# Optimization experiments

Hardware: AMD Instinct MI355X
Metric: run time of the kernel (lower is better)

The kernel has to match this reference:

```python
import jax, jax.numpy as jnp
import numpy as np

NB_ATOMS = 128
NB_CH = 1
ATOM = 12          # atom_size
BATCH = 8
HW = 75            # -> 64x64 patch grid
LAM = 0.1          # soft-threshold level of the L1 proximal
UNROLL = 2         # unroll_steps
FISTA_ITERS = 15   # fixed inner FISTA iterations (replaces res-based stop)


def _prox(u):
    # soft-thresholding (prox of lam*||.||_1)
    return jnp.sign(u) * jnp.maximum(jnp.abs(u) - LAM, 0.0)


def _conv(x, w):
    # valid cross-correlation, NCHW / OIHW (== F.conv2d)
    return jax.lax.conv_general_dilated(x, w, (1, 1), 'VALID',
                                        dimension_numbers=('NCHW', 'OIHW', 'NCHW'))


def _fold(patches, H, W):
    # patches: [B, Ph, Pw, a, a] -> overlap-add to [B, 1, H, W] (== F.fold)
    B, Ph, Pw, a, _ = patches.shape
    out = jnp.zeros((B, H, W), patches.dtype)
    for di in range(a):              # fixed small kernel loop (a*a = 144 slots)
        for dj in range(a):
            out = out.at[:, di:di + Ph, dj:dj + Pw].add(patches[:, :, :, di, dj])
    return out[:, None]


def _fista(c0, X, q, mu):
    # standard FISTA on 0.5*||D^T c - y_patch||^2 + lam*||c||_1 with step mu
    def body(i, st):
        c, z, t = st
        cn = _prox(z - (z @ X - q) * mu)
        tn = (1.0 + jnp.sqrt(1.0 + 4.0 * t * t)) / 2.0
        zn = cn + ((t - 1.0) / tn) * (cn - c)
        return (cn, zn, tn)
    c, _, _ = jax.lax.fori_loop(0, FISTA_ITERS, body, (c0, c0, jnp.float32(1.0)))
    return c


def setup_inputs() -> dict:
    key = jax.random.key(0)
    k1, k2 = jax.random.split(key)
    y = jax.random.normal(k1, (BATCH, NB_CH, HW, HW), dtype=jnp.float32)
    atoms = jax.random.normal(k2, (NB_ATOMS, NB_CH, ATOM, ATOM), dtype=jnp.float32) / 1500.0
    beta = jnp.float32(0.1)
    mu = jnp.float32(1.0)
    return {"y": y, "atoms": atoms, "beta": beta, "mu": mu}


def reference(y, atoms, beta, mu):
    B, C, H, W = y.shape
    N, a = atoms.shape[0], atoms.shape[-1]
    beta = jax.nn.relu(beta)
    mu = jax.nn.relu(mu)
    # normalize atoms: zero-mean, unit L2 rows, then spectral norm / sqrt(mu)
    A = atoms - atoms.mean(axis=(1, 2, 3), keepdims=True)
    Af = A.reshape(N, -1)
    Af = Af / jnp.linalg.norm(Af, axis=1, keepdims=True)
    Af = Af / (jnp.linalg.norm(Af, ord=2) * jnp.sqrt(mu))
    atoms_n = Af.reshape(N, C, a, a)
    X = Af @ Af.T                                   # [N, N] gram
    Ph, Pw = H - a + 1, W - a + 1
    n_patch = B * Ph * Pw
    mean_filter = jnp.ones((1, 1, a, a), y.dtype) / (a * a)
    patch_mean = _conv(y, mean_filter).reshape(n_patch, 1, 1, 1)
    divisors = _fold(jnp.ones((B, Ph, Pw, a, a), y.dtype), H, W)  # overlap counts
    goal = y
    c = jnp.zeros((n_patch, N), y.dtype)
    sg = jax.lax.stop_gradient
    for _ in range(UNROLL):
        q = _conv(goal, atoms_n).transpose(0, 2, 3, 1).reshape(n_patch, N)
        cf = sg(_fista(sg(c), sg(X), sg(q), sg(mu)))   # torch.no_grad inner solve
        cf = _prox(cf - (cf @ X - q) * mu)             # one differentiable step
        pred = jnp.einsum('pn,ncij->pcij', cf, atoms_n) + patch_mean  # [P,1,a,a]
        pred = _fold(pred.reshape(B, Ph, Pw, a, a), H, W)
        goal = (y + beta * pred) / (1.0 + beta * divisors)
        c = cf
    return goal
```

## Files before the change

### kernel.cpp

```cpp
#include <hip/hip_runtime.h>
#include <stdint.h>

#define AA 144
#define LAM 0.1f

#define OFS_SC    0
#define OFS_AF1   64
#define OFS_G     36928
#define OFS_S0    53312
#define OFS_S1    69696
#define OFS_X     86080
#define OFS_PM    139328
#define OFS_GOAL  172096
#define OFS_CF    4411456
#define OFS_PRED  8605760
#define OFS_ATB   OFS_S0
#define OFS_ANTB  OFS_S1


typedef __attribute__((ext_vector_type(8))) short short8_t;
typedef __attribute__((ext_vector_type(4))) float f32x4;
typedef __attribute__((ext_vector_type(2))) float f32x2;
typedef __attribute__((ext_vector_type(4))) uint32_t u32x4;

__device__ __forceinline__ unsigned short f2bf(float f) {
    union { float f; uint32_t u; } x; x.f = f;
    uint32_t u = x.u;
    return (unsigned short)((u + 0x7FFFu + ((u >> 16) & 1u)) >> 16);
}
__device__ __forceinline__ unsigned short f2bh(float f) {
    union { float f; uint32_t u; } x; x.f = f;
    return (unsigned short)((x.u + 0x8000u) >> 16);
}
__device__ __forceinline__ float bf2f(unsigned short u) {
    union { float f; uint32_t i; } x; x.i = ((uint32_t)u) << 16; return x.f;
}
__device__ __forceinline__ uint32_t pack_bf(float a, float b) {
    union { float f; uint32_t u; } xa, xb; xa.f = a; xb.f = b;
    return __builtin_amdgcn_perm(xb.u + 0x8000u, xa.u + 0x8000u, 0x07060302u);
}
__device__ __forceinline__ uint32_t cvt_pk(float a, float b) {
    uint32_t r;
    asm("v_cvt_pk_bf16_f32 %0, %1, %2" : "=v"(r) : "v"(a), "v"(b));
    return r;
}

#define PSTR 136
__global__ __launch_bounds__(1024) void k_setup(const float* atoms, const float* mu_p,
                                                float* ws, const float* y) {
    __shared__ unsigned short ABf[128 * 168];
    __shared__ unsigned short Pb[2][128 * PSTR];
    __shared__ float tr_arr[10];
    __shared__ float v[128];
    __shared__ float red[256];
    int t = threadIdx.x;
    if (blockIdx.x != 0) {
        int e = (blockIdx.x - 1) * 1024 + t;
        if (e < 45000) ws[OFS_GOAL + e] = y[e];
        if (e < 32768) {
            int b = e >> 12, pi = (e >> 6) & 63, pj = e & 63;
            const float* yb = y + b * 5625;
            float s = 0.f;
            for (int di = 0; di < 12; ++di) {
                const float* row = yb + (pi + di) * 75 + pj;
                #pragma unroll
                for (int dj = 0; dj < 12; ++dj) s += row[dj];
            }
            ws[OFS_PM + e] = s * (1.0f / 144.0f);
        }
        return;
    }
    int lane = t & 63, w = t >> 6;
    int col = lane & 15, quad = lane >> 4;
    if (t < 10) tr_arr[t] = (t == 0) ? 128.0f : 0.f;

    {
        int a = t >> 3, sub = t & 7;
        const float* ap = atoms + a * AA + sub * 18;
        float s = 0.f;
        #pragma unroll
        for (int k = 0; k < 18; ++k) s += ap[k];
        s += __shfl_xor(s, 1, 8); s += __shfl_xor(s, 2, 8); s += __shfl_xor(s, 4, 8);
        float mean = s * (1.0f / 144.0f);
        float ss = 0.f;
        #pragma unroll
        for (int k = 0; k < 18; ++k) { float d = ap[k] - mean; ss = fmaf(d, d, ss); }
        ss += __shfl_xor(ss, 1, 8); ss += __shfl_xor(ss, 2, 8); ss += __shfl_xor(ss, 4, 8);
        float rn = 1.0f / sqrtf(ss);
        #pragma unroll
        for (int k = 0; k < 18; ++k) {
            float av = (ap[k] - mean) * rn;
            ws[OFS_AF1 + a * AA + sub * 18 + k] = av;
            ABf[a * 168 + sub * 18 + k] = f2bf(av);
        }
        if (sub == 0) {
            #pragma unroll
            for (int k = AA; k < 160; ++k) ABf[a * 168 + k] = 0;
        }
    }
    __syncthreads();

    {
        uint32_t* D32 = (uint32_t*)Pb[0];
        float* G = ws + OFS_G;
        int mt = w & 7, gh = w >> 3;
        short8_t af[5];
        #pragma unroll
        for (int s = 0; s < 5; ++s)
            af[s] = *(const short8_t*)&ABf[(mt * 16 + col) * 168 + s * 32 + quad * 8];
        #pragma unroll
        for (int gi = 0; gi < 2; ++gi) {
            int g = gh * 2 + gi;
            short8_t b0[5], b1[5];
            #pragma unroll
            for (int s = 0; s < 5; ++s) {
                b0[s] = *(const short8_t*)&ABf[((2 * g) * 16 + col) * 168 + s * 32 + quad * 8];
                b1[s] = *(const short8_t*)&ABf[((2 * g + 1) * 16 + col) * 168 + s * 32 + quad * 8];
            }
            f32x4 a0 = (f32x4){0.f, 0.f, 0.f, 0.f};
            f32x4 a1 = (f32x4){0.f, 0.f, 0.f, 0.f};
            #pragma unroll
            for (int s = 0; s < 5; ++s) {
                a0 = __builtin_amdgcn_mfma_f32_16x16x32_bf16(af[s], b0[s], a0, 0, 0, 0);
                a1 = __builtin_amdgcn_mfma_f32_16x16x32_bf16(af[s], b1[s], a1, 0, 0, 0);
            }
            #pragma unroll
            for (int r = 0; r < 4; ++r) {
                int m = mt * 16 + quad * 4 + r;
                G[m * 128 + g * 32 + col] = a0[r];
                G[m * 128 + g * 32 + 16 + col] = a1[r];
                D32[m * 68 + g * 16 + col] = pack_bf(a0[r], a1[r]);
            }
        }
    }
    __syncthreads();

    int cur = 0;
    #pragma unroll 1
    for (int j = 0; j < 8; ++j) {
        float trn = tr_arr[j];
        float inv2 = 1.0f / (trn * trn);
        const unsigned short* S = Pb[cur];
        uint32_t* D32 = (uint32_t*)Pb[cur ^ 1];
        int mt = w & 7, nh = w >> 3;
        short8_t af[4];
        #pragma unroll
        for (int s = 0; s < 4; ++s)
            af[s] = *(const short8_t*)&S[(mt * 16 + col) * PSTR + s * 32 + quad * 8];
        #pragma unroll
        for (int pr = 0; pr < 2; ++pr) {
            int ntE = 4 * nh + 2 * pr, ntO = ntE + 1;
            short8_t bE[4], bO[4];
            #pragma unroll
            for (int s = 0; s < 4; ++s) {
                bE[s] = *(const short8_t*)&S[(ntE * 16 + col) * PSTR + s * 32 + quad * 8];
                bO[s] = *(const short8_t*)&S[(ntO * 16 + col) * PSTR + s * 32 + quad * 8];
            }
            f32x4 aE = (f32x4){0.f, 0.f, 0.f, 0.f};
            f32x4 aO = (f32x4){0.f, 0.f, 0.f, 0.f};
            #pragma unroll
            for (int s = 0; s < 4; ++s) {
                aE = __builtin_amdgcn_mfma_f32_16x16x32_bf16(af[s], bE[s], aE, 0, 0, 0);
                aO = __builtin_amdgcn_mfma_f32_16x16x32_bf16(af[s], bO[s], aO, 0, 0, 0);
            }
            int nE = ntE * 16 + col, nO = ntO * 16 + col;
            #pragma unroll
            for (int r = 0; r < 4; ++r) {
                float x0 = aE[r] * inv2, x1 = aO[r] * inv2;
                int row = mt * 16 + quad * 4 + r;
                D32[row * 68 + (ntE >> 1) * 16 + col] = pack_bf(x0, x1);
                if (row == nE) atomicAdd(&tr_arr[j + 1], x0);
                if (row == nO) atomicAdd(&tr_arr[j + 1], x1);
            }
        }
        __syncthreads();
        cur ^= 1;
    }

    {
        int a = t >> 3, sub = t & 7;
        const unsigned short* S = Pb[cur];
        float s = 0.f;
        #pragma unroll
        for (int k = 0; k < 16; ++k) s += bf2f(S[a * PSTR + sub * 16 + k]);
        s += __shfl_xor(s, 1, 8); s += __shfl_xor(s, 2, 8); s += __shfl_xor(s, 4, 8);
        if (sub == 0) v[a] = s;
    }
    __syncthreads();
    {
        int a = t >> 3, sub = t & 7;
        const float* G = ws + OFS_G;
        float wv = 0.f;
        #pragma unroll
        for (int k = 0; k < 16; ++k)
            wv = fmaf(G[a * 128 + sub * 16 + k], v[sub * 16 + k], wv);
        wv += __shfl_xor(wv, 1, 8); wv += __shfl_xor(wv, 2, 8); wv += __shfl_xor(wv, 4, 8);
        if (sub == 0) { red[a] = v[a] * wv; red[128 + a] = v[a] * v[a]; }
    }
    __syncthreads();
    for (int off = 64; off > 0; off >>= 1) {
        if (t < off) { red[t] += red[t + off]; red[128 + t] += red[128 + t + off]; }
        __syncthreads();
    }
    if (t == 0) {
        float lam = red[0] / red[128];
        float mu = fmaxf(mu_p[0], 0.0f);
        float scX = 1.0f / (lam * mu);
        float scA = 1.0f / (sqrtf(lam) * sqrtf(mu));
        ws[OFS_SC + 16] = scX * mu;
        ws[OFS_SC + 17] = scA;
        ws[OFS_SC + 18] = -scA * mu;
    }
}

__global__ __launch_bounds__(256) void k_finalize(float* ws) {
    int idx = blockIdx.x * 256 + threadIdx.x;
    float scX = ws[OFS_SC + 16], scA = ws[OFS_SC + 17], scQ = ws[OFS_SC + 18];
    if (idx < 16384) {
        int row = idx >> 7, ks = idx & 127;
        int s = ks >> 5, Q = (ks >> 3) & 3, j = ks & 7;
        int n = 32 * s + 16 * (j >> 2) + 4 * Q + (j & 3);
        ((unsigned short*)(ws + OFS_X))[idx] = f2bf(ws[OFS_G + row * 128 + n] * scX);
    } else if (idx < 36864) {
        int e = idx - 16384;
        int n = e / 160, k = e - n * 160;
        float v = (k < 144) ? ws[OFS_AF1 + n * 144 + k] * scQ : 0.f;
        ((unsigned short*)(ws + OFS_ATB))[e] = f2bf(v);
    } else {
        int e = idx - 36864;
        int jr = e >> 7, ks = e & 127;
        int s = ks >> 5, Q = (ks >> 3) & 3, j = ks & 7;
        int n = 32 * s + 16 * (j >> 2) + 4 * Q + (j & 3);
        ((unsigned short*)(ws + OFS_ANTB))[e] = f2bf(ws[OFS_AF1 + n * 144 + jr] * scA);
    }
}

__global__ __launch_bounds__(64, 1) void k_fista(const unsigned short* XPB,
        const float* goal, const unsigned short* ATB, const unsigned short* ANTBP,
        const float* pm, uint32_t* cfgb, unsigned short* predh,
        int first, int write_cf) {
    int lane = threadIdx.x & 63;
    int col = lane & 15, Q = lane >> 4;
    int wid = blockIdx.x;
    int b = wid >> 8, pi = (wid >> 2) & 63;
    int pcol = (wid & 3) * 16 + col;
    int p = wid * 16 + col;
    const float* gb = goal + b * 5625 + pi * 75;

    u32x4 bq[5];
    #pragma unroll
    for (int s = 0; s < 5; ++s)
        #pragma unroll
        for (int jj = 0; jj < 4; ++jj) {
            int k0 = 32 * s + 8 * Q + 2 * jj;
            float v0 = 0.f, v1 = 0.f;
            if (k0 < 144) {
                int di = k0 / 12, dj = k0 - di * 12;
                const float* r = gb + di * 75 + pcol + dj;
                v0 = r[0]; v1 = r[1];
            }
            bq[s][jj] = cvt_pk(v0, v1);
        }

    f32x4 qn4[8];
    #pragma unroll
    for (int m = 0; m < 8; ++m) {
        short8_t af[5];
        #pragma unroll
        for (int s = 0; s < 5; ++s)
            af[s] = *(const short8_t*)&ATB[(m * 16 + col) * 160 + 32 * s + 8 * Q];
        f32x4 a = (f32x4){0.f, 0.f, 0.f, 0.f};
        #pragma unroll
        for (int s = 0; s < 5; ++s)
            a = __builtin_amdgcn_mfma_f32_16x16x32_bf16(af[s],
                    __builtin_bit_cast(short8_t, bq[s]), a, 0, 0, 0);
        qn4[m] = a;
    }

    short8_t xf[8][4];
    #pragma unroll
    for (int m = 0; m < 8; ++m)
        #pragma unroll
        for (int s = 0; s < 4; ++s)
            xf[m][s] = *(const short8_t*)&XPB[(m * 16 + col) * 128 + 32 * s + 8 * Q];

    f32x4 c4[8], z4[8], acc4[8];
    u32x4 bfr[4];
    if (first) {
        #pragma unroll
        for (int m = 0; m < 8; ++m) c4[m] = z4[m] = (f32x4){0.f, 0.f, 0.f, 0.f};
        #pragma unroll
        for (int s = 0; s < 4; ++s) bfr[s] = (u32x4){0u, 0u, 0u, 0u};
    } else {
        const u32x4* cp = (const u32x4*)(cfgb + ((size_t)wid * 64 + lane) * 16);
        #pragma unroll
        for (int s = 0; s < 4; ++s) {
            u32x4 v = cp[s];
            bfr[s] = v;
            #pragma unroll
            for (int jj = 0; jj < 4; ++jj) {
                int m = (s << 1) | (jj >> 1), r = 2 * (jj & 1);
                uint32_t pk = v[jj];
                c4[m][r]     = __builtin_bit_cast(float, pk << 16);
                c4[m][r + 1] = __builtin_bit_cast(float, pk & 0xFFFF0000u);
            }
        }
        #pragma unroll
        for (int m = 0; m < 8; ++m) z4[m] = c4[m];
    }

    const f32x4 lamP = (f32x4){LAM, LAM, LAM, LAM};
    const f32x4 lamN = (f32x4){-LAM, -LAM, -LAM, -LAM};

    auto matmul = [&]() {
        #pragma unroll
        for (int m = 0; m < 8; ++m)
            acc4[m] = __builtin_amdgcn_mfma_f32_16x16x32_bf16(xf[m][0],
                          __builtin_bit_cast(short8_t, bfr[0]), qn4[m], 0, 0, 0);
        #pragma unroll
        for (int s = 1; s < 4; ++s)
            #pragma unroll
            for (int m = 0; m < 8; ++m)
                acc4[m] = __builtin_amdgcn_mfma_f32_16x16x32_bf16(xf[m][s],
                              __builtin_bit_cast(short8_t, bfr[s]), acc4[m], 0, 0, 0);
    };
    auto pack = [&](f32x4 (&src)[8]) {
        #pragma unroll
        for (int s = 0; s < 4; ++s)
            #pragma unroll
            for (int jj = 0; jj < 4; ++jj) {
                int m = (s << 1) | (jj >> 1), r = 2 * (jj & 1);
                bfr[s][jj] = cvt_pk(src[m][r], src[m][r + 1]);
            }
    };

    float tm = 1.0f;
    #pragma unroll 2
    for (int it = 0; it < 14; ++it) {
        matmul();
        float tn = 0.5f * (1.0f + sqrtf(1.0f + 4.0f * tm * tm));
        float fm = (tm - 1.0f) / tn;
        tm = tn;
        f32x4 fm4 = (f32x4){fm, fm, fm, fm};
        #pragma unroll
        for (int m = 0; m < 8; ++m) {
            f32x4 u = z4[m] - acc4[m];
            f32x4 cl = __builtin_elementwise_min(__builtin_elementwise_max(u, lamN), lamP);
            f32x4 cn = u - cl;
            z4[m] = cn + fm4 * (cn - c4[m]);
            c4[m] = cn;
        }
        pack(z4);
    }
    {
        matmul();
        #pragma unroll
        for (int m = 0; m < 8; ++m) {
            f32x4 u = z4[m] - acc4[m];
            f32x4 cl = __builtin_elementwise_min(__builtin_elementwise_max(u, lamN), lamP);
            c4[m] = u - cl;
        }
        pack(c4);
    }
    {
        matmul();
        #pragma unroll
        for (int m = 0; m < 8; ++m) {
            f32x4 u = c4[m] - acc4[m];
            f32x4 cl = __builtin_elementwise_min(__builtin_elementwise_max(u, lamN), lamP);
            c4[m] = u - cl;
        }
        pack(c4);
    }
    if (write_cf) {
        u32x4* cp = (u32x4*)(cfgb + ((size_t)wid * 64 + lane) * 16);
        #pragma unroll
        for (int s = 0; s < 4; ++s) cp[s] = bfr[s];
    }

    {
        float pmv = pm[p];
        f32x4 pm4 = (f32x4){pmv, pmv, pmv, pmv};
        #pragma unroll
        for (int jm = 0; jm < 9; ++jm) {
            short8_t anf[4];
            #pragma unroll
            for (int s = 0; s < 4; ++s)
                anf[s] = *(const short8_t*)&ANTBP[(jm * 16 + col) * 128 + 32 * s + 8 * Q];
            f32x4 a = pm4;
            #pragma unroll
            for (int s = 0; s < 4; ++s)
                a = __builtin_amdgcn_mfma_f32_16x16x32_bf16(anf[s],
                        __builtin_bit_cast(short8_t, bfr[s]), a, 0, 0, 0);
            #pragma unroll
            for (int r = 0; r < 4; ++r)
                predh[(jm * 16 + 4 * Q + r) * 32768 + p] = f2bh(a[r]);
        }
    }
}

__global__ __launch_bounds__(256) void k_fold(const float* y, const float* beta_p,
                                              const unsigned short* predh, float* goal,
                                              float* out, int write_out) {
    __shared__ float P[12 * 832];
    int i = blockIdx.x, b = blockIdx.y;
    int t = threadIdx.x;
    for (int di = 0; di < 12; ++di) {
        int pi = i - di;
        if ((unsigned)pi >= 64u) continue;
        int base = (b << 12) + (pi << 6);
        #pragma unroll
        for (int it = 0; it < 3; ++it) {
            int e = t + it * 256;
            int dj = e >> 6, pj = e & 63;
            P[di * 832 + pj * 13 + dj] = bf2f(predh[(di * 12 + dj) * 32768 + base + pj]);
        }
    }
    __syncthreads();
    if (t >= 75) return;
    int j = t;
    float S = 0.f;
    for (int di = 0; di < 12; ++di) {
        if ((unsigned)(i - di) >= 64u) continue;
        const float* Pd = &P[di * 832];
        #pragma unroll
        for (int dj = 0; dj < 12; ++dj) {
            int pj = j - dj;
            if ((unsigned)pj >= 64u) continue;
            S += Pd[pj * 13 + dj];
        }
    }
    int ci = min(i, 11) - max(i - 63, 0) + 1;
    int cj = min(j, 11) - max(j - 63, 0) + 1;
    float beta = fmaxf(beta_p[0], 0.0f);
    int idx = i * 75 + j;
    float yv = y[b * 5625 + idx];
    float g = (yv + beta * S) / (1.0f + beta * (float)(ci * cj));
    if (write_out) out[b * 5625 + idx] = g;
    else           goal[b * 5625 + idx] = g;
}

extern "C" void kernel_launch(void* const* d_in, const int* in_sizes, int n_in,
                              void* d_out, int out_size, void* d_ws, size_t ws_size,
                              hipStream_t stream) {
    const float* y     = (const float*)d_in[0];
    const float* atoms = (const float*)d_in[1];
    const float* beta  = (const float*)d_in[2];
    const float* mu    = (const float*)d_in[3];
    float* out = (float*)d_out;
    float* ws = (float*)d_ws;

    k_setup<<<46, 1024, 0, stream>>>(atoms, mu, ws, y);
    k_finalize<<<216, 256, 0, stream>>>(ws);

    for (int u = 0; u < 2; ++u) {
        k_fista<<<2048, 64, 0, stream>>>((const unsigned short*)(ws + OFS_X),
                                         ws + OFS_GOAL,
                                         (const unsigned short*)(ws + OFS_ATB),
                                         (const unsigned short*)(ws + OFS_ANTB),
                                         ws + OFS_PM, (uint32_t*)(ws + OFS_CF),
                                         (unsigned short*)(ws + OFS_PRED),
                                         u == 0 ? 1 : 0, u == 0 ? 1 : 0);
        k_fold<<<dim3(75, 8), 256, 0, stream>>>(y, beta,
                                                (const unsigned short*)(ws + OFS_PRED),
                                                ws + OFS_GOAL, out, u == 1 ? 1 : 0);
    }
}
```

Before: 204.1 us.

## Split FISTA atom rows across two waves with LDS exchange of iterates

Each FISTA block now runs two wavefronts, each owning half of the 128 atom rows of the Gram matvec, and the two halves exchange the packed bf16 iterate through double-buffered shared memory with a barrier every iteration. This halves per-wave MFMA work and register footprint (allowing more resident waves), and the prediction GEMM is split 5/4 across the waves. The soft-threshold clamp is switched to fmed3. The cost is a __syncthreads and LDS round trip per iteration on the serial dependency chain.

```diff
diff --git a/kernel.cpp b/kernel.cpp
--- a/kernel.cpp
+++ b/kernel.cpp
@@ -235,16 +235,18 @@
     }
 }
 
-__global__ __launch_bounds__(64, 1) void k_fista(const unsigned short* XPB,
+__global__ __launch_bounds__(128, 3) void k_fista(const unsigned short* XPB,
         const float* goal, const unsigned short* ATB, const unsigned short* ANTBP,
         const float* pm, uint32_t* cfgb, unsigned short* predh,
         int first, int write_cf) {
-    int lane = threadIdx.x & 63;
+    __shared__ u32x4 Zx[2][2][2][64];
+    int t = threadIdx.x;
+    int lane = t & 63, w = t >> 6;
     int col = lane & 15, Q = lane >> 4;
-    int wid = blockIdx.x;
-    int b = wid >> 8, pi = (wid >> 2) & 63;
-    int pcol = (wid & 3) * 16 + col;
-    int p = wid * 16 + col;
+    int blk = blockIdx.x;
+    int b = blk >> 8, pi = (blk >> 2) & 63;
+    int pcol = (blk & 3) * 16 + col;
+    int p = blk * 16 + col;
     const float* gb = goal + b * 5625 + pi * 75;
 
     u32x4 bq[5];
@@ -262,13 +264,13 @@
             bq[s][jj] = cvt_pk(v0, v1);
         }
 
-    f32x4 qn4[8];
+    f32x4 qn4[4];
     #pragma unroll
-    for (int m = 0; m < 8; ++m) {
+    for (int m = 0; m < 4; ++m) {
         short8_t af[5];
         #pragma unroll
         for (int s = 0; s < 5; ++s)
-            af[s] = *(const short8_t*)&ATB[(m * 16 + col) * 160 + 32 * s + 8 * Q];
+            af[s] = *(const short8_t*)&ATB[((w * 4 + m) * 16 + col) * 160 + 32 * s + 8 * Q];
         f32x4 a = (f32x4){0.f, 0.f, 0.f, 0.f};
         #pragma unroll
         for (int s = 0; s < 5; ++s)
@@ -277,61 +279,67 @@
         qn4[m] = a;
     }
 
-    short8_t xf[8][4];
+    short8_t xf[4][4];
     #pragma unroll
-    for (int m = 0; m < 8; ++m)
+    for (int m = 0; m < 4; ++m)
         #pragma unroll
         for (int s = 0; s < 4; ++s)
-            xf[m][s] = *(const short8_t*)&XPB[(m * 16 + col) * 128 + 32 * s + 8 * Q];
-
-    f32x4 c4[8], z4[8], acc4[8];
+            xf[m][s] = *(const short8_t*)&XPB[((w * 4 + m) * 16 + col) * 128 + 32 * s + 8 * Q];
+
+    f32x4 c4[4], z4[4], acc4[4];
     u32x4 bfr[4];
     if (first) {
         #pragma unroll
-        for (int m = 0; m < 8; ++m) c4[m] = z4[m] = (f32x4){0.f, 0.f, 0.f, 0.f};
+        for (int m = 0; m < 4; ++m) c4[m] = z4[m] = (f32x4){0.f, 0.f, 0.f, 0.f};
         #pragma unroll
         for (int s = 0; s < 4; ++s) bfr[s] = (u32x4){0u, 0u, 0u, 0u};
     } else {
-        const u32x4* cp = (const u32x4*)(cfgb + ((size_t)wid * 64 + lane) * 16);
-        #pragma unroll
-        for (int s = 0; s < 4; ++s) {
-            u32x4 v = cp[s];
-            bfr[s] = v;
+        const u32x4* cp = (const u32x4*)(cfgb + ((size_t)blk * 64 + lane) * 16);
+        #pragma unroll
+        for (int s = 0; s < 4; ++s) bfr[s] = cp[s];
+        #pragma unroll
+        for (int sp = 0; sp < 2; ++sp) {
+            u32x4 v = bfr[2 * w + sp];
             #pragma unroll
             for (int jj = 0; jj < 4; ++jj) {
-                int m = (s << 1) | (jj >> 1), r = 2 * (jj & 1);
+                int m = (sp << 1) | (jj >> 1), r = 2 * (jj & 1);
                 uint32_t pk = v[jj];
                 c4[m][r]     = __builtin_bit_cast(float, pk << 16);
                 c4[m][r + 1] = __builtin_bit_cast(float, pk & 0xFFFF0000u);
             }
         }
         #pragma unroll
-        for (int m = 0; m < 8; ++m) z4[m] = c4[m];
-    }
-
-    const f32x4 lamP = (f32x4){LAM, LAM, LAM, LAM};
-    const f32x4 lamN = (f32x4){-LAM, -LAM, -LAM, -LAM};
+        for (int m = 0; m < 4; ++m) z4[m] = c4[m];
+    }
 
     auto matmul = [&]() {
         #pragma unroll
-        for (int m = 0; m < 8; ++m)
+        for (int m = 0; m < 4; ++m)
             acc4[m] = __builtin_amdgcn_mfma_f32_16x16x32_bf16(xf[m][0],
                           __builtin_bit_cast(short8_t, bfr[0]), qn4[m], 0, 0, 0);
         #pragma unroll
         for (int s = 1; s < 4; ++s)
             #pragma unroll
-            for (int m = 0; m < 8; ++m)
+            for (int m = 0; m < 4; ++m)
                 acc4[m] = __builtin_amdgcn_mfma_f32_16x16x32_bf16(xf[m][s],
                               __builtin_bit_cast(short8_t, bfr[s]), acc4[m], 0, 0, 0);
     };
-    auto pack = [&](f32x4 (&src)[8]) {
-        #pragma unroll
-        for (int s = 0; s < 4; ++s)
+    auto pack = [&](f32x4 (&src)[4]) {
+        #pragma unroll
+        for (int sp = 0; sp < 2; ++sp)
             #pragma unroll
             for (int jj = 0; jj < 4; ++jj) {
-                int m = (s << 1) | (jj >> 1), r = 2 * (jj & 1);
-                bfr[s][jj] = cvt_pk(src[m][r], src[m][r + 1]);
-            }
+                int m = (sp << 1) | (jj >> 1), r = 2 * (jj & 1);
+                bfr[2 * w + sp][jj] = cvt_pk(src[m][r], src[m][r + 1]);
+            }
+    };
+    int ow = w ^ 1;
+    auto exchange = [&](int buf) {
+        Zx[buf][w][0][lane] = bfr[2 * w];
+        Zx[buf][w][1][lane] = bfr[2 * w + 1];
+        __syncthreads();
+        bfr[2 * ow]     = Zx[buf][ow][0][lane];
+        bfr[2 * ow + 1] = Zx[buf][ow][1][lane];
     };
 
     float tm = 1.0f;
@@ -343,58 +351,71 @@
         tm = tn;
         f32x4 fm4 = (f32x4){fm, fm, fm, fm};
         #pragma unroll
-        for (int m = 0; m < 8; ++m) {
+        for (int m = 0; m < 4; ++m) {
             f32x4 u = z4[m] - acc4[m];
-            f32x4 cl = __builtin_elementwise_min(__builtin_elementwise_max(u, lamN), lamP);
+            f32x4 cl;
+            #pragma unroll
+            for (int e = 0; e < 4; ++e) cl[e] = __builtin_amdgcn_fmed3f(u[e], -LAM, LAM);
             f32x4 cn = u - cl;
             z4[m] = cn + fm4 * (cn - c4[m]);
             c4[m] = cn;
         }
         pack(z4);
+        exchange(it & 1);
     }
     {
         matmul();
         #pragma unroll
-        for (int m = 0; m < 8; ++m) {
+        for (int m = 0; m < 4; ++m) {
             f32x4 u = z4[m] - acc4[m];
-            f32x4 cl = __builtin_elementwise_min(__builtin_elementwise_max(u, lamN), lamP);
+            f32x4 cl;
+            #pragma unroll
+            for (int e = 0; e < 4; ++e) cl[e] = __builtin_amdgcn_fmed3f(u[e], -LAM, LAM);
             c4[m] = u - cl;
         }
         pack(c4);
+        exchange(0);
     }
     {
         matmul();
         #pragma unroll
-        for (int m = 0; m < 8; ++m) {
+        for (int m = 0; m < 4; ++m) {
             f32x4 u = c4[m] - acc4[m];
-            f32x4 cl = __builtin_elementwise_min(__builtin_elementwise_max(u, lamN), lamP);
+            f32x4 cl;
+            #pragma unroll
+            for (int e = 0; e < 4; ++e) cl[e] = __builtin_amdgcn_fmed3f(u[e], -LAM, LAM);
             c4[m] = u - cl;
         }
         pack(c4);
+        exchange(1);
     }
     if (write_cf) {
-        u32x4* cp = (u32x4*)(cfgb + ((size_t)wid * 64 + lane) * 16);
-        #pragma unroll
-        for (int s = 0; s < 4; ++s) cp[s] = bfr[s];
+        u32x4* cp = (u32x4*)(cfgb + ((size_t)blk * 64 + lane) * 16);
+        cp[2 * w]     = bfr[2 * w];
+        cp[2 * w + 1] = bfr[2 * w + 1];
     }
 
     {
         float pmv = pm[p];
         f32x4 pm4 = (f32x4){pmv, pmv, pmv, pmv};
-        #pragma unroll
-        for (int jm = 0; jm < 9; ++jm) {
-            short8_t anf[4];
-            #pragma unroll
-            for (int s = 0; s < 4; ++s)
-                anf[s] = *(const short8_t*)&ANTBP[(jm * 16 + col) * 128 + 32 * s + 8 * Q];
-            f32x4 a = pm4;
-            #pragma unroll
-            for (int s = 0; s < 4; ++s)
-                a = __builtin_amdgcn_mfma_f32_16x16x32_bf16(anf[s],
-                        __builtin_bit_cast(short8_t, bfr[s]), a, 0, 0, 0);
-            #pragma unroll
-            for (int r = 0; r < 4; ++r)
-                predh[(jm * 16 + 4 * Q + r) * 32768 + p] = f2bh(a[r]);
+        int jm0 = w ? 5 : 0, jmN = w ? 4 : 5;
+        #pragma unroll
+        for (int ji = 0; ji < 5; ++ji) {
+            if (ji < jmN) {
+                int jm = jm0 + ji;
+                short8_t anf[4];
+                #pragma unroll
+                for (int s = 0; s < 4; ++s)
+                    anf[s] = *(const short8_t*)&ANTBP[(jm * 16 + col) * 128 + 32 * s + 8 * Q];
+                f32x4 a = pm4;
+                #pragma unroll
+                for (int s = 0; s < 4; ++s)
+                    a = __builtin_amdgcn_mfma_f32_16x16x32_bf16(anf[s],
+                            __builtin_bit_cast(short8_t, bfr[s]), a, 0, 0, 0);
+                #pragma unroll
+                for (int r = 0; r < 4; ++r)
+                    predh[(jm * 16 + 4 * Q + r) * 32768 + p] = f2bh(a[r]);
+            }
         }
     }
 }
@@ -454,13 +475,13 @@
     k_finalize<<<216, 256, 0, stream>>>(ws);
 
     for (int u = 0; u < 2; ++u) {
-        k_fista<<<2048, 64, 0, stream>>>((const unsigned short*)(ws + OFS_X),
-                                         ws + OFS_GOAL,
-                                         (const unsigned short*)(ws + OFS_ATB),
-                                         (const unsigned short*)(ws + OFS_ANTB),
-                                         ws + OFS_PM, (uint32_t*)(ws + OFS_CF),
-                                         (unsigned short*)(ws + OFS_PRED),
-                                         u == 0 ? 1 : 0, u == 0 ? 1 : 0);
+        k_fista<<<2048, 128, 0, stream>>>((const unsigned short*)(ws + OFS_X),
+                                          ws + OFS_GOAL,
+                                          (const unsigned short*)(ws + OFS_ATB),
+                                          (const unsigned short*)(ws + OFS_ANTB),
+                                          ws + OFS_PM, (uint32_t*)(ws + OFS_CF),
+                                          (unsigned short*)(ws + OFS_PRED),
+                                          u == 0 ? 1 : 0, u == 0 ? 1 : 0);
         k_fold<<<dim3(75, 8), 256, 0, stream>>>(y, beta,
                                                 (const unsigned short*)(ws + OFS_PRED),
                                                 ws + OFS_GOAL, out, u == 1 ? 1 : 0);
```

Measured after the change: 322.1 us. +57.8%, slower.
